# Optimization experiments

Hardware: AMD Instinct MI355X
Metric: run time of the kernel (lower is better)

Reference implementation:

```python
import jax, jax.numpy as jnp
import numpy as np

B, S, D, H = 4, 2048, 512, 8
DK = D // H  # 64


def setup_inputs() -> dict:
    key = jax.random.key(0)
    ks = jax.random.split(key, 7)
    return {
        "q": jax.random.normal(ks[0], (B, S, D), dtype=jnp.float32),
        "k": jax.random.normal(ks[1], (B, S, D), dtype=jnp.float32),
        "v": jax.random.normal(ks[2], (B, S, D), dtype=jnp.float32),
        # per-head query projection weights (also used for k and v, replicating
        # the source's bug where q_linear projects all three inputs)
        "Wq": jax.random.normal(ks[3], (H, DK, D), dtype=jnp.float32) * (1.0 / np.sqrt(D)),
        "bq": jax.random.normal(ks[4], (H, DK), dtype=jnp.float32) * 0.02,
        "Wout": jax.random.normal(ks[5], (D, H * DK), dtype=jnp.float32) * (1.0 / np.sqrt(D)),
        "bout": jax.random.normal(ks[6], (D,), dtype=jnp.float32) * 0.02,
    }


def reference(q, k, v, Wq, bq, Wout, bout):
    # Per-head projections, batched over heads. NOTE: the original module
    # (buggy but faithful) applies the SAME q_linear to q, k and v.
    scale = 1.0 / jnp.sqrt(jnp.asarray(Wq.shape[1], dtype=q.dtype))
    qh = jnp.einsum("bsd,hed->bhse", q, Wq) + bq[:, None, :]  # [B,H,S,DK]
    kh = jnp.einsum("bsd,hed->bhse", k, Wq) + bq[:, None, :]
    vh = jnp.einsum("bsd,hed->bhse", v, Wq) + bq[:, None, :]
    scores = jnp.einsum("bhqe,bhke->bhqk", qh, kh) * scale  # [B,H,S,S]
    weights = jax.nn.softmax(scores, axis=-1)
    heads = jnp.einsum("bhqk,bhke->bhqe", weights, vh)  # [B,H,S,DK]
    # concat heads along feature dim (head-major order matches torch.cat)
    concat = heads.transpose(0, 2, 1, 3).reshape(q.shape[0], q.shape[1], -1)
    return concat @ Wout.T + bout
```

## Files before the change

kernel.cpp:

```cpp
#include <hip/hip_runtime.h>

#define BB 4
#define SS 2048
#define DD 512
#define HH 8
#define DKK 64
#define HDK 512

typedef __attribute__((ext_vector_type(4))) float f32x4;
typedef __attribute__((ext_vector_type(8))) __bf16 bf16x8;
typedef __attribute__((ext_vector_type(4))) __bf16 bf16x4;

#define MFMA16(a, b, c) __builtin_amdgcn_mfma_f32_16x16x32_bf16((a), (b), (c), 0, 0, 0)

__global__ __launch_bounds__(256) void proj_kernel(
    const float* __restrict__ q, const float* __restrict__ k, const float* __restrict__ v,
    const float* __restrict__ Wq, const float* __restrict__ bq,
    __bf16* __restrict__ qh, __bf16* __restrict__ kh, __bf16* __restrict__ vt)
{
    const int z  = blockIdx.z;
    const float* X = (z == 0) ? q : (z == 1) ? k : v;
    const int m0 = blockIdx.x * 64;
    const int n0 = blockIdx.y * 64;

    __shared__ __align__(16) __bf16 As[64][72];
    __shared__ __align__(16) __bf16 Bs[64][72];

    const int t    = threadIdx.x;
    const int lane = t & 63, wid = t >> 6;
    const int lo   = lane & 15, hi = lane >> 4;
    const int wm   = wid >> 1, wn = wid & 1;

    f32x4 acc[2][2] = {};

    for (int k0 = 0; k0 < DD; k0 += 64) {
        __syncthreads();
        {
            const int row = t >> 4;
            const int col = (t & 15) * 4;
#pragma unroll
            for (int i = 0; i < 4; ++i) {
                const int r = row + i * 16;
                float4 a = *reinterpret_cast<const float4*>(&X[(size_t)(m0 + r) * DD + k0 + col]);
                bf16x4 ta = {(__bf16)a.x, (__bf16)a.y, (__bf16)a.z, (__bf16)a.w};
                *reinterpret_cast<bf16x4*>(&As[r][col]) = ta;
                float4 b = *reinterpret_cast<const float4*>(&Wq[(size_t)(n0 + r) * DD + k0 + col]);
                bf16x4 tb = {(__bf16)b.x, (__bf16)b.y, (__bf16)b.z, (__bf16)b.w};
                *reinterpret_cast<bf16x4*>(&Bs[r][col]) = tb;
            }
        }
        __syncthreads();
#pragma unroll
        for (int kk = 0; kk < 2; ++kk) {
            bf16x8 a[2], b[2];
#pragma unroll
            for (int mi = 0; mi < 2; ++mi)
                a[mi] = *reinterpret_cast<const bf16x8*>(&As[wm * 32 + mi * 16 + lo][kk * 32 + hi * 8]);
#pragma unroll
            for (int ni = 0; ni < 2; ++ni)
                b[ni] = *reinterpret_cast<const bf16x8*>(&Bs[wn * 32 + ni * 16 + lo][kk * 32 + hi * 8]);
#pragma unroll
            for (int mi = 0; mi < 2; ++mi)
#pragma unroll
                for (int ni = 0; ni < 2; ++ni)
                    acc[mi][ni] = MFMA16(a[mi], b[ni], acc[mi][ni]);
        }
    }

#pragma unroll
    for (int mi = 0; mi < 2; ++mi) {
#pragma unroll
        for (int ni = 0; ni < 2; ++ni) {
            const int n = n0 + wn * 32 + ni * 16 + lo;
            const float bias = bq[n];
            const int h_ = n >> 6, e_ = n & 63;
#pragma unroll
            for (int r = 0; r < 4; ++r) {
                const int m = m0 + wm * 32 + mi * 16 + hi * 4 + r;
                const float val = acc[mi][ni][r] + bias;
                const int b_ = m >> 11, s_ = m & (SS - 1);
                const size_t bh = (size_t)(b_ * HH + h_);
                if (z == 0)
                    qh[(bh * SS + s_) * DKK + e_] = (__bf16)val;
                else if (z == 1)
                    kh[(bh * SS + s_) * DKK + e_] = (__bf16)val;
                else
                    vt[(bh * DKK + e_) * SS + s_] = (__bf16)val;
            }
        }
    }
}

__global__ __launch_bounds__(256) void attn_kernel(
    const __bf16* __restrict__ qh, const __bf16* __restrict__ kh,
    const __bf16* __restrict__ vt, __bf16* __restrict__ concat)
{
    const int q0 = blockIdx.x * 128;
    const int bh = blockIdx.y;
    const int b_ = bh >> 3, h_ = bh & 7;
    const size_t base = (size_t)bh * SS * DKK;
    const __bf16* qhp = qh + base;
    const __bf16* khp = kh + base;
    const __bf16* vtp = vt + base;

    const int t    = threadIdx.x;
    const int lane = t & 63, wid = t >> 6;
    const int lo   = lane & 15, hi = lane >> 4;

    __shared__ __align__(16) __bf16 Ks[64 * 64];
    __shared__ __align__(16) __bf16 Vts[64 * 64];
    __shared__ __align__(16) __bf16 Ps[4][32][72];

    char* KsB  = (char*)Ks;
    char* VtsB = (char*)Vts;

    const int sr  = lane >> 3;
    const int gcb = (lane & 7) << 4;
    const int scb = gcb ^ (sr << 4);
    const int srow = 16 * wid + sr;

    bf16x8 qf[2][2];
#pragma unroll
    for (int g = 0; g < 2; ++g)
#pragma unroll
        for (int kk = 0; kk < 2; ++kk)
            qf[g][kk] = *reinterpret_cast<const bf16x8*>(
                &qhp[(size_t)(q0 + 32 * wid + 16 * g + lo) * DKK + 32 * kk + 8 * hi]);

    f32x4 acc[4][2] = {};
    float m_run[2] = {-INFINITY, -INFINITY};
    float l_run[2] = {0.f, 0.f};

    for (int kv0 = 0; kv0 < SS; kv0 += 64) {
        bf16x8 kr0 = *reinterpret_cast<const bf16x8*>(
            (const char*)&khp[(size_t)(kv0 + srow) * DKK] + gcb);
        bf16x8 kr1 = *reinterpret_cast<const bf16x8*>(
            (const char*)&khp[(size_t)(kv0 + srow + 8) * DKK] + gcb);
        bf16x8 vr0 = *reinterpret_cast<const bf16x8*>(
            (const char*)&vtp[(size_t)srow * SS + kv0] + gcb);
        bf16x8 vr1 = *reinterpret_cast<const bf16x8*>(
            (const char*)&vtp[(size_t)(srow + 8) * SS + kv0] + gcb);

        __syncthreads();
        *reinterpret_cast<bf16x8*>(KsB  + srow * 128 + scb)       = kr0;
        *reinterpret_cast<bf16x8*>(KsB  + (srow + 8) * 128 + scb) = kr1;
        *reinterpret_cast<bf16x8*>(VtsB + srow * 128 + scb)       = vr0;
        *reinterpret_cast<bf16x8*>(VtsB + (srow + 8) * 128 + scb) = vr1;
        __syncthreads();

        f32x4 sc[4][2] = {};
#pragma unroll
        for (int kk = 0; kk < 2; ++kk) {
            bf16x8 kf[4];
#pragma unroll
            for (int f = 0; f < 4; ++f) {
                const int row = 16 * f + lo;
                const int cb  = (64 * kk + 16 * hi) ^ ((row & 7) << 4);
                kf[f] = *reinterpret_cast<const bf16x8*>(KsB + row * 128 + cb);
            }
#pragma unroll
            for (int f = 0; f < 4; ++f)
#pragma unroll
                for (int g = 0; g < 2; ++g)
                    sc[f][g] = MFMA16(kf[f], qf[g][kk], sc[f][g]);
        }

#pragma unroll
        for (int g = 0; g < 2; ++g) {
            float mx = -1e30f;
#pragma unroll
            for (int f = 0; f < 4; ++f)
#pragma unroll
                for (int r = 0; r < 4; ++r)
                    mx = fmaxf(mx, sc[f][g][r]);
            mx = fmaxf(mx, __shfl_xor(mx, 16));
            mx = fmaxf(mx, __shfl_xor(mx, 32));
            mx *= 0.125f;
            const float mnew = fmaxf(m_run[g], mx);
            const float scl  = __expf(m_run[g] - mnew);
            float rs = 0.f;
#pragma unroll
            for (int f = 0; f < 4; ++f) {
                bf16x4 pk;
#pragma unroll
                for (int r = 0; r < 4; ++r) {
                    const float e = __expf(sc[f][g][r] * 0.125f - mnew);
                    rs += e;
                    pk[r] = (__bf16)e;
                }
                *reinterpret_cast<bf16x4*>(&Ps[wid][16 * g + lo][16 * f + 4 * hi]) = pk;
            }
            rs += __shfl_xor(rs, 16);
            rs += __shfl_xor(rs, 32);
            l_run[g] = l_run[g] * scl + rs;
            m_run[g] = mnew;
#pragma unroll
            for (int f = 0; f < 4; ++f)
                acc[f][g] *= scl;
        }

#pragma unroll
        for (int kk = 0; kk < 2; ++kk) {
            bf16x8 pb[2];
#pragma unroll
            for (int g = 0; g < 2; ++g)
                pb[g] = *reinterpret_cast<const bf16x8*>(&Ps[wid][16 * g + lo][32 * kk + 8 * hi]);
#pragma unroll
            for (int f = 0; f < 4; ++f) {
                const int row = 16 * f + lo;
                const int cb  = (64 * kk + 16 * hi) ^ ((row & 7) << 4);
                bf16x8 vf = *reinterpret_cast<const bf16x8*>(VtsB + row * 128 + cb);
#pragma unroll
                for (int g = 0; g < 2; ++g)
                    acc[f][g] = MFMA16(vf, pb[g], acc[f][g]);
            }
        }
    }

#pragma unroll
    for (int g = 0; g < 2; ++g) {
        const float inv = 1.0f / l_run[g];
        const int qrow = q0 + 32 * wid + 16 * g + lo;
        const size_t ob = ((size_t)b_ * SS + qrow) * HDK + h_ * DKK;
#pragma unroll
        for (int f = 0; f < 4; ++f) {
            bf16x4 o;
#pragma unroll
            for (int r = 0; r < 4; ++r)
                o[r] = (__bf16)(acc[f][g][r] * inv);
            *reinterpret_cast<bf16x4*>(&concat[ob + 16 * f + 4 * hi]) = o;
        }
    }
}

__global__ __launch_bounds__(256) void outproj_kernel(
    const __bf16* __restrict__ concat, const float* __restrict__ Wout,
    const float* __restrict__ bout, float* __restrict__ out)
{
    const int m0 = blockIdx.x * 64;
    const int n0 = blockIdx.y * 64;

    __shared__ __align__(16) __bf16 As[64][72];
    __shared__ __align__(16) __bf16 Bs[64][72];

    const int t    = threadIdx.x;
    const int lane = t & 63, wid = t >> 6;
    const int lo   = lane & 15, hi = lane >> 4;
    const int wm   = wid >> 1, wn = wid & 1;

    f32x4 acc[2][2] = {};

    for (int k0 = 0; k0 < HDK; k0 += 64) {
        __syncthreads();
        {
            const int arow = t >> 3, acol = (t & 7) * 8;
#pragma unroll
            for (int i = 0; i < 2; ++i) {
                const int r = arow + i * 32;
                *reinterpret_cast<bf16x8*>(&As[r][acol]) =
                    *reinterpret_cast<const bf16x8*>(&concat[(size_t)(m0 + r) * HDK + k0 + acol]);
            }
            const int row = t >> 4, col = (t & 15) * 4;
#pragma unroll
            for (int i = 0; i < 4; ++i) {
                const int r = row + i * 16;
                float4 b = *reinterpret_cast<const float4*>(&Wout[(size_t)(n0 + r) * HDK + k0 + col]);
                bf16x4 tb = {(__bf16)b.x, (__bf16)b.y, (__bf16)b.z, (__bf16)b.w};
                *reinterpret_cast<bf16x4*>(&Bs[r][col]) = tb;
            }
        }
        __syncthreads();
#pragma unroll
        for (int kk = 0; kk < 2; ++kk) {
            bf16x8 a[2], b[2];
#pragma unroll
            for (int mi = 0; mi < 2; ++mi)
                a[mi] = *reinterpret_cast<const bf16x8*>(&As[wm * 32 + mi * 16 + lo][kk * 32 + hi * 8]);
#pragma unroll
            for (int ni = 0; ni < 2; ++ni)
                b[ni] = *reinterpret_cast<const bf16x8*>(&Bs[wn * 32 + ni * 16 + lo][kk * 32 + hi * 8]);
#pragma unroll
            for (int mi = 0; mi < 2; ++mi)
#pragma unroll
                for (int ni = 0; ni < 2; ++ni)
                    acc[mi][ni] = MFMA16(a[mi], b[ni], acc[mi][ni]);
        }
    }

#pragma unroll
    for (int mi = 0; mi < 2; ++mi) {
#pragma unroll
        for (int ni = 0; ni < 2; ++ni) {
            const int n = n0 + wn * 32 + ni * 16 + lo;
            const float bias = bout[n];
#pragma unroll
            for (int r = 0; r < 4; ++r) {
                const int m = m0 + wm * 32 + mi * 16 + hi * 4 + r;
                out[(size_t)m * DD + n] = acc[mi][ni][r] + bias;
            }
        }
    }
}

extern "C" void kernel_launch(void* const* d_in, const int* in_sizes, int n_in,
                              void* d_out, int out_size, void* d_ws, size_t ws_size,
                              hipStream_t stream)
{
    (void)in_sizes; (void)n_in; (void)out_size; (void)ws_size;
    const float* q    = (const float*)d_in[0];
    const float* k    = (const float*)d_in[1];
    const float* v    = (const float*)d_in[2];
    const float* Wq   = (const float*)d_in[3];
    const float* bq   = (const float*)d_in[4];
    const float* Wout = (const float*)d_in[5];
    const float* bout = (const float*)d_in[6];
    float* out = (float*)d_out;

    char* ws = (char*)d_ws;
    __bf16* qh = (__bf16*)(ws);
    __bf16* kh = (__bf16*)(ws + (8u << 20));
    __bf16* vt = (__bf16*)(ws + (16u << 20));
    __bf16* cc = (__bf16*)(ws + (24u << 20));

    proj_kernel<<<dim3(BB * SS / 64, HDK / 64, 3), 256, 0, stream>>>(q, k, v, Wq, bq, qh, kh, vt);
    attn_kernel<<<dim3(SS / 128, BB * HH), 256, 0, stream>>>(qh, kh, vt, cc);
    outproj_kernel<<<dim3(BB * SS / 64, DD / 64), 256, 0, stream>>>(cc, Wout, bout, out);
}
```

Before: 236.4 us.

## Enlarge GEMM tiles to 128x128 with swizzled LDS and halve attention query tile

Both projection GEMMs move from 64x64 to 128x128 block tiles with 4x4 MFMA fragments per wave. Global loads are issued into registers before the barrier, and LDS uses an XOR swizzle in place of padding. The attention kernel drops to 64 queries per block (16 per wave), which doubles the grid. The GEMM changes aim to increase operand reuse and cut global traffic; the attention change aims to raise occupancy and parallelism, but it loads each K/V tile twice as often and raises register pressure in the GEMMs.

```diff
diff --git a/kernel.cpp b/kernel.cpp
--- a/kernel.cpp
+++ b/kernel.cpp
@@ -12,6 +12,13 @@
 typedef __attribute__((ext_vector_type(4))) __bf16 bf16x4;
 
 #define MFMA16(a, b, c) __builtin_amdgcn_mfma_f32_16x16x32_bf16((a), (b), (c), 0, 0, 0)
+
+__device__ inline bf16x8 cvt8(const float4 a, const float4 b) {
+    bf16x8 w;
+    w[0] = (__bf16)a.x; w[1] = (__bf16)a.y; w[2] = (__bf16)a.z; w[3] = (__bf16)a.w;
+    w[4] = (__bf16)b.x; w[5] = (__bf16)b.y; w[6] = (__bf16)b.z; w[7] = (__bf16)b.w;
+    return w;
+}
 
 __global__ __launch_bounds__(256) void proj_kernel(
     const float* __restrict__ q, const float* __restrict__ k, const float* __restrict__ v,
@@ -20,63 +27,80 @@
 {
     const int z  = blockIdx.z;
     const float* X = (z == 0) ? q : (z == 1) ? k : v;
-    const int m0 = blockIdx.x * 64;
-    const int n0 = blockIdx.y * 64;
-
-    __shared__ __align__(16) __bf16 As[64][72];
-    __shared__ __align__(16) __bf16 Bs[64][72];
+    const int m0 = blockIdx.x * 128;
+    const int n0 = blockIdx.y * 128;
+
+    __shared__ __align__(16) __bf16 As[128 * 64];
+    __shared__ __align__(16) __bf16 Bs[128 * 64];
+    char* AsB = (char*)As;
+    char* BsB = (char*)Bs;
 
     const int t    = threadIdx.x;
     const int lane = t & 63, wid = t >> 6;
     const int lo   = lane & 15, hi = lane >> 4;
     const int wm   = wid >> 1, wn = wid & 1;
 
-    f32x4 acc[2][2] = {};
+    const int srow  = t >> 1;
+    const int shalf = (t & 1) * 32;
+    const int sswz  = (srow & 7) << 4;
+
+    f32x4 acc[4][4] = {};
 
     for (int k0 = 0; k0 < DD; k0 += 64) {
-        __syncthreads();
-        {
-            const int row = t >> 4;
-            const int col = (t & 15) * 4;
-#pragma unroll
-            for (int i = 0; i < 4; ++i) {
-                const int r = row + i * 16;
-                float4 a = *reinterpret_cast<const float4*>(&X[(size_t)(m0 + r) * DD + k0 + col]);
-                bf16x4 ta = {(__bf16)a.x, (__bf16)a.y, (__bf16)a.z, (__bf16)a.w};
-                *reinterpret_cast<bf16x4*>(&As[r][col]) = ta;
-                float4 b = *reinterpret_cast<const float4*>(&Wq[(size_t)(n0 + r) * DD + k0 + col]);
-                bf16x4 tb = {(__bf16)b.x, (__bf16)b.y, (__bf16)b.z, (__bf16)b.w};
-                *reinterpret_cast<bf16x4*>(&Bs[r][col]) = tb;
-            }
-        }
-        __syncthreads();
+        float4 xa[8], xb[8];
+#pragma unroll
+        for (int i = 0; i < 8; ++i) {
+            xa[i] = *reinterpret_cast<const float4*>(&X [(size_t)(m0 + srow) * DD + k0 + shalf + 4 * i]);
+            xb[i] = *reinterpret_cast<const float4*>(&Wq[(size_t)(n0 + srow) * DD + k0 + shalf + 4 * i]);
+        }
+        bf16x8 wa[4], wb[4];
+#pragma unroll
+        for (int j = 0; j < 4; ++j) {
+            wa[j] = cvt8(xa[2 * j], xa[2 * j + 1]);
+            wb[j] = cvt8(xb[2 * j], xb[2 * j + 1]);
+        }
+        __syncthreads();
+#pragma unroll
+        for (int j = 0; j < 4; ++j) {
+            const int cb = ((shalf + 8 * j) * 2) ^ sswz;
+            *reinterpret_cast<bf16x8*>(AsB + srow * 128 + cb) = wa[j];
+            *reinterpret_cast<bf16x8*>(BsB + srow * 128 + cb) = wb[j];
+        }
+        __syncthreads();
+
 #pragma unroll
         for (int kk = 0; kk < 2; ++kk) {
-            bf16x8 a[2], b[2];
-#pragma unroll
-            for (int mi = 0; mi < 2; ++mi)
-                a[mi] = *reinterpret_cast<const bf16x8*>(&As[wm * 32 + mi * 16 + lo][kk * 32 + hi * 8]);
-#pragma unroll
-            for (int ni = 0; ni < 2; ++ni)
-                b[ni] = *reinterpret_cast<const bf16x8*>(&Bs[wn * 32 + ni * 16 + lo][kk * 32 + hi * 8]);
-#pragma unroll
-            for (int mi = 0; mi < 2; ++mi)
-#pragma unroll
-                for (int ni = 0; ni < 2; ++ni)
+            bf16x8 a[4], b[4];
+#pragma unroll
+            for (int mi = 0; mi < 4; ++mi) {
+                const int row = wm * 64 + mi * 16 + lo;
+                a[mi] = *reinterpret_cast<const bf16x8*>(
+                    AsB + row * 128 + ((kk * 64 + hi * 16) ^ ((row & 7) << 4)));
+            }
+#pragma unroll
+            for (int ni = 0; ni < 4; ++ni) {
+                const int row = wn * 64 + ni * 16 + lo;
+                b[ni] = *reinterpret_cast<const bf16x8*>(
+                    BsB + row * 128 + ((kk * 64 + hi * 16) ^ ((row & 7) << 4)));
+            }
+#pragma unroll
+            for (int mi = 0; mi < 4; ++mi)
+#pragma unroll
+                for (int ni = 0; ni < 4; ++ni)
                     acc[mi][ni] = MFMA16(a[mi], b[ni], acc[mi][ni]);
         }
     }
 
 #pragma unroll
-    for (int mi = 0; mi < 2; ++mi) {
-#pragma unroll
-        for (int ni = 0; ni < 2; ++ni) {
-            const int n = n0 + wn * 32 + ni * 16 + lo;
+    for (int mi = 0; mi < 4; ++mi) {
+#pragma unroll
+        for (int ni = 0; ni < 4; ++ni) {
+            const int n = n0 + wn * 64 + ni * 16 + lo;
             const float bias = bq[n];
             const int h_ = n >> 6, e_ = n & 63;
 #pragma unroll
             for (int r = 0; r < 4; ++r) {
-                const int m = m0 + wm * 32 + mi * 16 + hi * 4 + r;
+                const int m = m0 + wm * 64 + mi * 16 + hi * 4 + r;
                 const float val = acc[mi][ni][r] + bias;
                 const int b_ = m >> 11, s_ = m & (SS - 1);
                 const size_t bh = (size_t)(b_ * HH + h_);
@@ -95,7 +119,7 @@
     const __bf16* __restrict__ qh, const __bf16* __restrict__ kh,
     const __bf16* __restrict__ vt, __bf16* __restrict__ concat)
 {
-    const int q0 = blockIdx.x * 128;
+    const int q0 = blockIdx.x * 64;
     const int bh = blockIdx.y;
     const int b_ = bh >> 3, h_ = bh & 7;
     const size_t base = (size_t)bh * SS * DKK;
@@ -109,27 +133,24 @@
 
     __shared__ __align__(16) __bf16 Ks[64 * 64];
     __shared__ __align__(16) __bf16 Vts[64 * 64];
-    __shared__ __align__(16) __bf16 Ps[4][32][72];
+    __shared__ __align__(16) __bf16 Ps[4][16][72];
 
     char* KsB  = (char*)Ks;
     char* VtsB = (char*)Vts;
 
-    const int sr  = lane >> 3;
-    const int gcb = (lane & 7) << 4;
-    const int scb = gcb ^ (sr << 4);
+    const int sr   = lane >> 3;
+    const int gcb  = (lane & 7) << 4;
+    const int scb  = gcb ^ (sr << 4);
     const int srow = 16 * wid + sr;
 
-    bf16x8 qf[2][2];
-#pragma unroll
-    for (int g = 0; g < 2; ++g)
-#pragma unroll
-        for (int kk = 0; kk < 2; ++kk)
-            qf[g][kk] = *reinterpret_cast<const bf16x8*>(
-                &qhp[(size_t)(q0 + 32 * wid + 16 * g + lo) * DKK + 32 * kk + 8 * hi]);
-
-    f32x4 acc[4][2] = {};
-    float m_run[2] = {-INFINITY, -INFINITY};
-    float l_run[2] = {0.f, 0.f};
+    bf16x8 qf[2];
+#pragma unroll
+    for (int kk = 0; kk < 2; ++kk)
+        qf[kk] = *reinterpret_cast<const bf16x8*>(
+            &qhp[(size_t)(q0 + 16 * wid + lo) * DKK + 32 * kk + 8 * hi]);
+
+    f32x4 acc[4] = {};
+    float m_run = -INFINITY, l_run = 0.f;
 
     for (int kv0 = 0; kv0 < SS; kv0 += 64) {
         bf16x8 kr0 = *reinterpret_cast<const bf16x8*>(
@@ -148,7 +169,7 @@
         *reinterpret_cast<bf16x8*>(VtsB + (srow + 8) * 128 + scb) = vr1;
         __syncthreads();
 
-        f32x4 sc[4][2] = {};
+        f32x4 sc[4] = {};
 #pragma unroll
         for (int kk = 0; kk < 2; ++kk) {
             bf16x8 kf[4];
@@ -160,74 +181,64 @@
             }
 #pragma unroll
             for (int f = 0; f < 4; ++f)
-#pragma unroll
-                for (int g = 0; g < 2; ++g)
-                    sc[f][g] = MFMA16(kf[f], qf[g][kk], sc[f][g]);
-        }
-
-#pragma unroll
-        for (int g = 0; g < 2; ++g) {
+                sc[f] = MFMA16(kf[f], qf[kk], sc[f]);
+        }
+
+        {
             float mx = -1e30f;
 #pragma unroll
             for (int f = 0; f < 4; ++f)
 #pragma unroll
                 for (int r = 0; r < 4; ++r)
-                    mx = fmaxf(mx, sc[f][g][r]);
+                    mx = fmaxf(mx, sc[f][r]);
             mx = fmaxf(mx, __shfl_xor(mx, 16));
             mx = fmaxf(mx, __shfl_xor(mx, 32));
-            mx *= 0.125f;
-            const float mnew = fmaxf(m_run[g], mx);
-            const float scl  = __expf(m_run[g] - mnew);
+            const float mnew = fmaxf(m_run, mx * 0.125f);
+            const float scl  = __expf(m_run - mnew);
             float rs = 0.f;
 #pragma unroll
             for (int f = 0; f < 4; ++f) {
                 bf16x4 pk;
 #pragma unroll
                 for (int r = 0; r < 4; ++r) {
-                    const float e = __expf(sc[f][g][r] * 0.125f - mnew);
+                    const float e = __expf(fmaf(sc[f][r], 0.125f, -mnew));
                     rs += e;
                     pk[r] = (__bf16)e;
                 }
-                *reinterpret_cast<bf16x4*>(&Ps[wid][16 * g + lo][16 * f + 4 * hi]) = pk;
+                *reinterpret_cast<bf16x4*>(&Ps[wid][lo][16 * f + 4 * hi]) = pk;
             }
             rs += __shfl_xor(rs, 16);
             rs += __shfl_xor(rs, 32);
-            l_run[g] = l_run[g] * scl + rs;
-            m_run[g] = mnew;
+            l_run = l_run * scl + rs;
+            m_run = mnew;
 #pragma unroll
             for (int f = 0; f < 4; ++f)
-                acc[f][g] *= scl;
+                acc[f] *= scl;
         }
 
 #pragma unroll
         for (int kk = 0; kk < 2; ++kk) {
-            bf16x8 pb[2];
-#pragma unroll
-            for (int g = 0; g < 2; ++g)
-                pb[g] = *reinterpret_cast<const bf16x8*>(&Ps[wid][16 * g + lo][32 * kk + 8 * hi]);
+            bf16x8 pb = *reinterpret_cast<const bf16x8*>(&Ps[wid][lo][32 * kk + 8 * hi]);
 #pragma unroll
             for (int f = 0; f < 4; ++f) {
                 const int row = 16 * f + lo;
                 const int cb  = (64 * kk + 16 * hi) ^ ((row & 7) << 4);
                 bf16x8 vf = *reinterpret_cast<const bf16x8*>(VtsB + row * 128 + cb);
-#pragma unroll
-                for (int g = 0; g < 2; ++g)
-                    acc[f][g] = MFMA16(vf, pb[g], acc[f][g]);
-            }
-        }
-    }
-
-#pragma unroll
-    for (int g = 0; g < 2; ++g) {
-        const float inv = 1.0f / l_run[g];
-        const int qrow = q0 + 32 * wid + 16 * g + lo;
+                acc[f] = MFMA16(vf, pb, acc[f]);
+            }
+        }
+    }
+
+    {
+        const float inv = 1.0f / l_run;
+        const int qrow = q0 + 16 * wid + lo;
         const size_t ob = ((size_t)b_ * SS + qrow) * HDK + h_ * DKK;
 #pragma unroll
         for (int f = 0; f < 4; ++f) {
             bf16x4 o;
 #pragma unroll
             for (int r = 0; r < 4; ++r)
-                o[r] = (__bf16)(acc[f][g][r] * inv);
+                o[r] = (__bf16)(acc[f][r] * inv);
             *reinterpret_cast<bf16x4*>(&concat[ob + 16 * f + 4 * hi]) = o;
         }
     }
@@ -237,65 +248,82 @@
     const __bf16* __restrict__ concat, const float* __restrict__ Wout,
     const float* __restrict__ bout, float* __restrict__ out)
 {
-    const int m0 = blockIdx.x * 64;
-    const int n0 = blockIdx.y * 64;
-
-    __shared__ __align__(16) __bf16 As[64][72];
-    __shared__ __align__(16) __bf16 Bs[64][72];
+    const int m0 = blockIdx.x * 128;
+    const int n0 = blockIdx.y * 128;
+
+    __shared__ __align__(16) __bf16 As[128 * 64];
+    __shared__ __align__(16) __bf16 Bs[128 * 64];
+    char* AsB = (char*)As;
+    char* BsB = (char*)Bs;
 
     const int t    = threadIdx.x;
     const int lane = t & 63, wid = t >> 6;
     const int lo   = lane & 15, hi = lane >> 4;
     const int wm   = wid >> 1, wn = wid & 1;
 
-    f32x4 acc[2][2] = {};
+    const int srow  = t >> 1;
+    const int shalf = (t & 1) * 32;
+    const int sswz  = (srow & 7) << 4;
+
+    f32x4 acc[4][4] = {};
 
     for (int k0 = 0; k0 < HDK; k0 += 64) {
-        __syncthreads();
-        {
-            const int arow = t >> 3, acol = (t & 7) * 8;
-#pragma unroll
-            for (int i = 0; i < 2; ++i) {
-                const int r = arow + i * 32;
-                *reinterpret_cast<bf16x8*>(&As[r][acol]) =
-                    *reinterpret_cast<const bf16x8*>(&concat[(size_t)(m0 + r) * HDK + k0 + acol]);
-            }
-            const int row = t >> 4, col = (t & 15) * 4;
-#pragma unroll
-            for (int i = 0; i < 4; ++i) {
-                const int r = row + i * 16;
-                float4 b = *reinterpret_cast<const float4*>(&Wout[(size_t)(n0 + r) * HDK + k0 + col]);
-                bf16x4 tb = {(__bf16)b.x, (__bf16)b.y, (__bf16)b.z, (__bf16)b.w};
-                *reinterpret_cast<bf16x4*>(&Bs[r][col]) = tb;
-            }
-        }
-        __syncthreads();
+        bf16x8 wa[4];
+#pragma unroll
+        for (int j = 0; j < 4; ++j)
+            wa[j] = *reinterpret_cast<const bf16x8*>(
+                &concat[(size_t)(m0 + srow) * HDK + k0 + shalf + 8 * j]);
+        float4 xb[8];
+#pragma unroll
+        for (int i = 0; i < 8; ++i)
+            xb[i] = *reinterpret_cast<const float4*>(
+                &Wout[(size_t)(n0 + srow) * HDK + k0 + shalf + 4 * i]);
+        bf16x8 wb[4];
+#pragma unroll
+        for (int j = 0; j < 4; ++j)
+            wb[j] = cvt8(xb[2 * j], xb[2 * j + 1]);
+
+        __syncthreads();
+#pragma unroll
+        for (int j = 0; j < 4; ++j) {
+            const int cb = ((shalf + 8 * j) * 2) ^ sswz;
+            *reinterpret_cast<bf16x8*>(AsB + srow * 128 + cb) = wa[j];
+            *reinterpret_cast<bf16x8*>(BsB + srow * 128 + cb) = wb[j];
+        }
+        __syncthreads();
+
 #pragma unroll
         for (int kk = 0; kk < 2; ++kk) {
-            bf16x8 a[2], b[2];
-#pragma unroll
-            for (int mi = 0; mi < 2; ++mi)
-                a[mi] = *reinterpret_cast<const bf16x8*>(&As[wm * 32 + mi * 16 + lo][kk * 32 + hi * 8]);
-#pragma unroll
-            for (int ni = 0; ni < 2; ++ni)
-                b[ni] = *reinterpret_cast<const bf16x8*>(&Bs[wn * 32 + ni * 16 + lo][kk * 32 + hi * 8]);
-#pragma unroll
-            for (int mi = 0; mi < 2; ++mi)
-#pragma unroll
-                for (int ni = 0; ni < 2; ++ni)
+            bf16x8 a[4], b[4];
+#pragma unroll
+            for (int mi = 0; mi < 4; ++mi) {
+                const int row = wm * 64 + mi * 16 + lo;
+                a[mi] = *reinterpret_cast<const bf16x8*>(
+                    AsB + row * 128 + ((kk * 64 + hi * 16) ^ ((row & 7) << 4)));
+            }
+#pragma unroll
+            for (int ni = 0; ni < 4; ++ni) {
+                const int row = wn * 64 + ni * 16 + lo;
+                b[ni] = *reinterpret_cast<const bf16x8*>(
+                    BsB + row * 128 + ((kk * 64 + hi * 16) ^ ((row & 7) << 4)));
+            }
+#pragma unroll
+            for (int mi = 0; mi < 4; ++mi)
+#pragma unroll
+                for (int ni = 0; ni < 4; ++ni)
                     acc[mi][ni] = MFMA16(a[mi], b[ni], acc[mi][ni]);
         }
     }
 
 #pragma unroll
-    for (int mi = 0; mi < 2; ++mi) {
-#pragma unroll
-        for (int ni = 0; ni < 2; ++ni) {
-            const int n = n0 + wn * 32 + ni * 16 + lo;
+    for (int mi = 0; mi < 4; ++mi) {
+#pragma unroll
+        for (int ni = 0; ni < 4; ++ni) {
+            const int n = n0 + wn * 64 + ni * 16 + lo;
             const float bias = bout[n];
 #pragma unroll
             for (int r = 0; r < 4; ++r) {
-                const int m = m0 + wm * 32 + mi * 16 + hi * 4 + r;
+                const int m = m0 + wm * 64 + mi * 16 + hi * 4 + r;
                 out[(size_t)m * DD + n] = acc[mi][ni][r] + bias;
             }
         }
@@ -322,7 +350,7 @@
     __bf16* vt = (__bf16*)(ws + (16u << 20));
     __bf16* cc = (__bf16*)(ws + (24u << 20));
 
-    proj_kernel<<<dim3(BB * SS / 64, HDK / 64, 3), 256, 0, stream>>>(q, k, v, Wq, bq, qh, kh, vt);
-    attn_kernel<<<dim3(SS / 128, BB * HH), 256, 0, stream>>>(qh, kh, vt, cc);
-    outproj_kernel<<<dim3(BB * SS / 64, DD / 64), 256, 0, stream>>>(cc, Wout, bout, out);
-}
+    proj_kernel<<<dim3(BB * SS / 128, HDK / 128, 3), 256, 0, stream>>>(q, k, v, Wq, bq, qh, kh, vt);
+    attn_kernel<<<dim3(SS / 64, BB * HH), 256, 0, stream>>>(qh, kh, vt, cc);
+    outproj_kernel<<<dim3(BB * SS / 128, DD / 128), 256, 0, stream>>>(cc, Wout, bout, out);
+}
```

Measured after the change: 244.0 us. +3.2%, slower.
